# Performance work log

Hardware: AMD Instinct MI355X
Metric: run time of the kernel (lower is better)

## Reference

```python
import jax, jax.numpy as jnp
import numpy as np

N_NODES = 50000
DEG = 16
N_EDGES = N_NODES * DEG  # 800000
C_IN = 64
C_OUT = 64


def setup_inputs() -> dict:
    key = jax.random.key(0)
    k_x, k_src, k_ea, k_w, k_b = jax.random.split(key, 5)
    x = jax.random.normal(k_x, (N_NODES, C_IN), dtype=jnp.float32)
    # Every node appears DEG times as a destination -> no empty segments in max-aggregation.
    dst = jnp.repeat(jnp.arange(N_NODES, dtype=jnp.int32), DEG)
    src = jax.random.randint(k_src, (N_EDGES,), 0, N_NODES, dtype=jnp.int32)
    edge_index = jnp.stack([src, dst], axis=0)  # [2, E], row0=source(j), row1=target(i)
    edge_attr = jax.random.normal(k_ea, (N_EDGES, 1), dtype=jnp.float32)  # unused by forward (faithful to source)
    # MLP(2*C_IN -> C_OUT): Linear weight [out, 2*in] + bias, kaiming-ish scale
    W = jax.random.normal(k_w, (C_OUT, 2 * C_IN), dtype=jnp.float32) * (1.0 / np.sqrt(2 * C_IN))
    b = jax.random.normal(k_b, (C_OUT,), dtype=jnp.float32) * 0.01
    return {"x": x, "edge_index": edge_index, "edge_attr": edge_attr, "W": W, "b": b}


def reference(x, edge_index, edge_attr, W, b):
    # PyG EdgeConv: out_i = max_{j in N(i)} MLP(concat(x_i, x_j - x_i)); aggr='max'
    src = edge_index[0]  # j (source)
    dst = edge_index[1]  # i (target)
    x_i = x[dst]                      # [E, C]
    x_j = x[src]                      # [E, C]
    feat = jnp.concatenate([x_i, x_j - x_i], axis=-1)   # [E, 2C]
    msg = jax.nn.relu(feat @ W.T + b)                    # [E, C_out] per-edge MLP
    out = jax.ops.segment_max(msg, dst, num_segments=x.shape[0])  # scatter-max
    # Guard against -inf for isolated nodes (none by construction, but match scatter fill=0)
    return jnp.where(jnp.isneginf(out), 0.0, out)
```

## Files before the change

### kernel.cpp

```cpp
#include <hip/hip_runtime.h>


#define DEG 16
#define C 64
#define NPW 8
#define WPB 4

typedef __attribute__((ext_vector_type(8))) short s16x8;
typedef __attribute__((ext_vector_type(4))) float f32x4;

__device__ __forceinline__ unsigned short f2bf(float f) {
    union { float f; unsigned u; } v; v.f = f;
    unsigned u = v.u + 0x7FFFu + ((v.u >> 16) & 1u);
    return (unsigned short)(u >> 16);
}


__global__ __launch_bounds__(256) void prep(const float* __restrict__ x,
                                            const float* __restrict__ W,
                                            unsigned short* __restrict__ ws_u,
                                            int n4) {
    int i = blockIdx.x * blockDim.x + threadIdx.x;
    if (i < n4) {
        f32x4 v = ((const f32x4*)x)[i];
        ushort4 o;
        o.x = f2bf(v[0]); o.y = f2bf(v[1]); o.z = f2bf(v[2]); o.w = f2bf(v[3]);
        ((ushort4*)ws_u)[i] = o;
    }
    if (blockIdx.x == 0 && threadIdx.x < 64) {
        const int lane = threadIdx.x, col = lane & 15, quad = lane >> 4;
        unsigned short* wf = ws_u + (size_t)n4 * 4;
        #pragma unroll
        for (int nt = 0; nt < 4; ++nt) {
            const float* wrow = W + (nt * 16 + col) * (2 * C);
            #pragma unroll
            for (int ks = 0; ks < 2; ++ks) {
                const int k0 = ks * 32 + quad * 8;
                f32x4 w1a = *(const f32x4*)(wrow + k0);
                f32x4 w1b = *(const f32x4*)(wrow + k0 + 4);
                f32x4 w2a = *(const f32x4*)(wrow + C + k0);
                f32x4 w2b = *(const f32x4*)(wrow + C + k0 + 4);
                s16x8 t2, td;
                #pragma unroll
                for (int j = 0; j < 4; ++j) {
                    t2[j]     = (short)f2bf(w2a[j]);
                    t2[j + 4] = (short)f2bf(w2b[j]);
                    td[j]     = (short)f2bf(w1a[j] - w2a[j]);
                    td[j + 4] = (short)f2bf(w1b[j] - w2b[j]);
                }
                *(s16x8*)(wf + (((0 * 8) + nt * 2 + ks) * 64 + lane) * 8) = td;
                *(s16x8*)(wf + (((1 * 8) + nt * 2 + ks) * 64 + lane) * 8) = t2;
            }
        }
    }
}

__global__ __launch_bounds__(256, 3) void edgeconv_mfma(
    const unsigned short* __restrict__ xb,
    const int* __restrict__ src,
    const float* __restrict__ bias,
    float* __restrict__ out,
    int n_groups, int n_nodes)
{
    const int lane = threadIdx.x & 63;
    const int wave = threadIdx.x >> 6;
    const int col  = lane & 15;
    const int quad = lane >> 4;
    int group = blockIdx.x * WPB + wave;
    if (group >= n_groups) group = n_groups - 1;
    const int node0 = group * NPW;

    int idx[NPW];
    #pragma unroll
    for (int n = 0; n < NPW; ++n)
        idx[n] = src[node0 * DEG + n * DEG + col];

    const unsigned short* wf = xb + (size_t)n_nodes * C;
    s16x8 bd[4][2], b2[4][2];
    #pragma unroll
    for (int nt = 0; nt < 4; ++nt)
        #pragma unroll
        for (int ks = 0; ks < 2; ++ks) {
            bd[nt][ks] = *(const s16x8*)(wf + ((nt * 2 + ks) * 64 + lane) * 8);
            b2[nt][ks] = *(const s16x8*)(wf + ((8 + nt * 2 + ks) * 64 + lane) * 8);
        }

    const int xirow = node0 + (col & 7);
    s16x8 xi0 = *(const s16x8*)(xb + xirow * C + quad * 8);
    s16x8 xi1 = *(const s16x8*)(xb + xirow * C + 32 + quad * 8);
    f32x4 baseD[4];
    #pragma unroll
    for (int nt = 0; nt < 4; ++nt) {
        float bv = bias[nt * 16 + col];
        baseD[nt] = (f32x4){bv, bv, bv, bv};
    }
    #pragma unroll
    for (int nt = 0; nt < 4; ++nt) {
        baseD[nt] = __builtin_amdgcn_mfma_f32_16x16x32_bf16(xi0, bd[nt][0], baseD[nt], 0, 0, 0);
        baseD[nt] = __builtin_amdgcn_mfma_f32_16x16x32_bf16(xi1, bd[nt][1], baseD[nt], 0, 0, 0);
    }

    s16x8 xa[NPW][2];
    #pragma unroll
    for (int n = 0; n < NPW; ++n) {
        xa[n][0] = *(const s16x8*)(xb + idx[n] * C + quad * 8);
        xa[n][1] = *(const s16x8*)(xb + idx[n] * C + 32 + quad * 8);
    }

    #pragma unroll
    for (int n = 0; n < NPW; ++n) {
        const int slane = ((n >> 2) << 4) | col;
        f32x4 acc[4];
        #pragma unroll
        for (int nt = 0; nt < 4; ++nt) {
            float bb = __shfl(baseD[nt][n & 3], slane);
            acc[nt] = (f32x4){bb, bb, bb, bb};
        }
        #pragma unroll
        for (int nt = 0; nt < 4; ++nt) {
            acc[nt] = __builtin_amdgcn_mfma_f32_16x16x32_bf16(xa[n][0], b2[nt][0], acc[nt], 0, 0, 0);
            acc[nt] = __builtin_amdgcn_mfma_f32_16x16x32_bf16(xa[n][1], b2[nt][1], acc[nt], 0, 0, 0);
        }
        float m[4];
        #pragma unroll
        for (int nt = 0; nt < 4; ++nt) {
            float t = fmaxf(fmaxf(acc[nt][0], acc[nt][1]),
                            fmaxf(acc[nt][2], acc[nt][3]));
            t = fmaxf(t, __shfl_xor(t, 16));
            t = fmaxf(t, __shfl_xor(t, 32));
            m[nt] = t;
        }
        float r = quad == 0 ? m[0] : quad == 1 ? m[1] : quad == 2 ? m[2] : m[3];
        r = fmaxf(r, 0.0f);
        out[(node0 + n) * C + lane] = r;
    }
}

__global__ __launch_bounds__(256, 2) void edgeconv_fallback(
    const float* __restrict__ x, const int* __restrict__ src,
    const float* __restrict__ W, const float* __restrict__ bias,
    float* __restrict__ out, int n_groups)
{
    const int lane = threadIdx.x & 63, wave = threadIdx.x >> 6;
    const int col = lane & 15, quad = lane >> 4;
    int group = blockIdx.x * WPB + wave;
    if (group >= n_groups) group = n_groups - 1;

    auto frag = [&](int row, int koff) {
        const float* p = x + row * C + koff;
        f32x4 a = *(const f32x4*)p, b = *(const f32x4*)(p + 4);
        s16x8 r;
        #pragma unroll
        for (int j = 0; j < 4; ++j) {
            r[j] = (short)f2bf(a[j]); r[j + 4] = (short)f2bf(b[j]);
        }
        return r;
    };

    s16x8 b2[4][2];
    f32x4 baseD[4];
    {
        s16x8 bd[4][2];
        #pragma unroll
        for (int nt = 0; nt < 4; ++nt) {
            const float* wrow = W + (nt * 16 + col) * (2 * C);
            #pragma unroll
            for (int ks = 0; ks < 2; ++ks) {
                const int k0 = ks * 32 + quad * 8;
                f32x4 w1a = *(const f32x4*)(wrow + k0);
                f32x4 w1b = *(const f32x4*)(wrow + k0 + 4);
                f32x4 w2a = *(const f32x4*)(wrow + C + k0);
                f32x4 w2b = *(const f32x4*)(wrow + C + k0 + 4);
                s16x8 t2, td;
                #pragma unroll
                for (int j = 0; j < 4; ++j) {
                    t2[j] = (short)f2bf(w2a[j]); t2[j + 4] = (short)f2bf(w2b[j]);
                    td[j] = (short)f2bf(w1a[j] - w2a[j]);
                    td[j + 4] = (short)f2bf(w1b[j] - w2b[j]);
                }
                b2[nt][ks] = t2; bd[nt][ks] = td;
            }
        }
        #pragma unroll
        for (int nt = 0; nt < 4; ++nt) {
            float bv = bias[nt * 16 + col];
            baseD[nt] = (f32x4){bv, bv, bv, bv};
        }
        const int nrow = group * 16 + col;
        s16x8 xi0 = frag(nrow, quad * 8), xi1 = frag(nrow, 32 + quad * 8);
        #pragma unroll
        for (int nt = 0; nt < 4; ++nt) {
            baseD[nt] = __builtin_amdgcn_mfma_f32_16x16x32_bf16(xi0, bd[nt][0], baseD[nt], 0, 0, 0);
            baseD[nt] = __builtin_amdgcn_mfma_f32_16x16x32_bf16(xi1, bd[nt][1], baseD[nt], 0, 0, 0);
        }
    }
    int idx[16];
    #pragma unroll
    for (int n = 0; n < 16; ++n) idx[n] = src[group * 256 + n * DEG + col];
    s16x8 xa[3][2];
    #pragma unroll
    for (int p = 0; p < 2; ++p) {
        xa[p][0] = frag(idx[p], quad * 8); xa[p][1] = frag(idx[p], 32 + quad * 8);
    }
    #pragma unroll
    for (int n = 0; n < 16; ++n) {
        if (n + 2 < 16) {
            xa[(n + 2) % 3][0] = frag(idx[n + 2], quad * 8);
            xa[(n + 2) % 3][1] = frag(idx[n + 2], 32 + quad * 8);
        }
        const int slane = ((n >> 2) << 4) | col;
        f32x4 acc[4];
        #pragma unroll
        for (int nt = 0; nt < 4; ++nt) {
            float bb = __shfl(baseD[nt][n & 3], slane);
            acc[nt] = (f32x4){bb, bb, bb, bb};
        }
        #pragma unroll
        for (int nt = 0; nt < 4; ++nt) {
            acc[nt] = __builtin_amdgcn_mfma_f32_16x16x32_bf16(xa[n % 3][0], b2[nt][0], acc[nt], 0, 0, 0);
            acc[nt] = __builtin_amdgcn_mfma_f32_16x16x32_bf16(xa[n % 3][1], b2[nt][1], acc[nt], 0, 0, 0);
        }
        float m[4];
        #pragma unroll
        for (int nt = 0; nt < 4; ++nt) {
            float t = fmaxf(fmaxf(acc[nt][0], acc[nt][1]),
                            fmaxf(acc[nt][2], acc[nt][3]));
            t = fmaxf(t, __shfl_xor(t, 16));
            t = fmaxf(t, __shfl_xor(t, 32));
            m[nt] = t;
        }
        float r = quad == 0 ? m[0] : quad == 1 ? m[1] : quad == 2 ? m[2] : m[3];
        out[(group * 16 + n) * C + lane] = fmaxf(r, 0.0f);
    }
}

extern "C" void kernel_launch(void* const* d_in, const int* in_sizes, int n_in,
                              void* d_out, int out_size, void* d_ws, size_t ws_size,
                              hipStream_t stream) {
    const float* x    = (const float*)d_in[0];
    const int*   src  = (const int*)  d_in[1];
    const float* W    = (const float*)d_in[3];
    const float* b    = (const float*)d_in[4];
    float*       out  = (float*)d_out;

    const int n_nodes = in_sizes[0] / C;
    const size_t need = ((size_t)n_nodes * C + 16 * 64 * 8) * sizeof(unsigned short);

    if (ws_size >= need) {
        unsigned short* ws_u = (unsigned short*)d_ws;
        const int n4 = n_nodes * C / 4;
        const int n_groups = (n_nodes + NPW - 1) / NPW;
        const int grid = (n_groups + WPB - 1) / WPB;
        prep<<<(n4 + 255) / 256, 256, 0, stream>>>(x, W, ws_u, n4);
        edgeconv_mfma<<<grid, 256, 0, stream>>>(ws_u, src, b, out, n_groups, n_nodes);
    } else {
        const int n_groups = (n_nodes + 15) / 16;
        edgeconv_fallback<<<(n_groups + WPB - 1) / WPB, 256, 0, stream>>>(
            x, src, W, b, out, n_groups);
    }
}
```

Measured before the change: 98.38 us.

## Precompute per-node linear projections, then gather-max fp16 rows per edge

Uses linearity: W2·x_j is computed once per node, and the base term (W1-W2)·x_i+b is computed once per destination, both stored as fp16. The edge stage then only gathers the projected source rows, takes an elementwise max, adds the base and applies relu, because relu(base + y) is monotone in y. This removes the per-edge MFMA work (16x redundant GEMM) and replaces it with a gather of 128-byte fp16 rows. It adds an fp16 rounding step on the intermediates, which may cost accuracy.

Result: slower. 104.6 us (+6.3%).

```diff
diff --git a/kernel.cpp b/kernel.cpp
--- a/kernel.cpp
+++ b/kernel.cpp
@@ -3,11 +3,12 @@
 
 #define DEG 16
 #define C 64
-#define NPW 8
 #define WPB 4
 
 typedef __attribute__((ext_vector_type(8))) short s16x8;
 typedef __attribute__((ext_vector_type(4))) float f32x4;
+typedef __attribute__((ext_vector_type(4))) int   i32x4;
+typedef _Float16 h8 __attribute__((ext_vector_type(8)));
 
 __device__ __forceinline__ unsigned short f2bf(float f) {
     union { float f; unsigned u; } v; v.f = f;
@@ -15,125 +16,135 @@
     return (unsigned short)(u >> 16);
 }
 
-
-__global__ __launch_bounds__(256) void prep(const float* __restrict__ x,
-                                            const float* __restrict__ W,
-                                            unsigned short* __restrict__ ws_u,
-                                            int n4) {
-    int i = blockIdx.x * blockDim.x + threadIdx.x;
-    if (i < n4) {
-        f32x4 v = ((const f32x4*)x)[i];
-        ushort4 o;
-        o.x = f2bf(v[0]); o.y = f2bf(v[1]); o.z = f2bf(v[2]); o.w = f2bf(v[3]);
-        ((ushort4*)ws_u)[i] = o;
-    }
-    if (blockIdx.x == 0 && threadIdx.x < 64) {
-        const int lane = threadIdx.x, col = lane & 15, quad = lane >> 4;
-        unsigned short* wf = ws_u + (size_t)n4 * 4;
-        #pragma unroll
-        for (int nt = 0; nt < 4; ++nt) {
-            const float* wrow = W + (nt * 16 + col) * (2 * C);
-            #pragma unroll
-            for (int ks = 0; ks < 2; ++ks) {
-                const int k0 = ks * 32 + quad * 8;
-                f32x4 w1a = *(const f32x4*)(wrow + k0);
-                f32x4 w1b = *(const f32x4*)(wrow + k0 + 4);
-                f32x4 w2a = *(const f32x4*)(wrow + C + k0);
-                f32x4 w2b = *(const f32x4*)(wrow + C + k0 + 4);
-                s16x8 t2, td;
-                #pragma unroll
-                for (int j = 0; j < 4; ++j) {
-                    t2[j]     = (short)f2bf(w2a[j]);
-                    t2[j + 4] = (short)f2bf(w2b[j]);
-                    td[j]     = (short)f2bf(w1a[j] - w2a[j]);
-                    td[j + 4] = (short)f2bf(w1b[j] - w2b[j]);
-                }
-                *(s16x8*)(wf + (((0 * 8) + nt * 2 + ks) * 64 + lane) * 8) = td;
-                *(s16x8*)(wf + (((1 * 8) + nt * 2 + ks) * 64 + lane) * 8) = t2;
-            }
-        }
-    }
-}
-
-__global__ __launch_bounds__(256, 3) void edgeconv_mfma(
-    const unsigned short* __restrict__ xb,
-    const int* __restrict__ src,
+__global__ __launch_bounds__(256) void prep_gemm(
+    const float* __restrict__ x, const float* __restrict__ W,
     const float* __restrict__ bias,
-    float* __restrict__ out,
+    _Float16* __restrict__ y, _Float16* __restrict__ base,
     int n_groups, int n_nodes)
 {
     const int lane = threadIdx.x & 63;
     const int wave = threadIdx.x >> 6;
     const int col  = lane & 15;
     const int quad = lane >> 4;
+    int g = blockIdx.x * WPB + wave;
+    if (g >= n_groups) g = n_groups - 1;
+
+    s16x8 bd[4][2], b2[4][2];
+    #pragma unroll
+    for (int nt = 0; nt < 4; ++nt) {
+        const float* wrow = W + (size_t)(nt * 16 + col) * (2 * C);
+        #pragma unroll
+        for (int ks = 0; ks < 2; ++ks) {
+            const int k0 = ks * 32 + quad * 8;
+            f32x4 w1a = *(const f32x4*)(wrow + k0);
+            f32x4 w1b = *(const f32x4*)(wrow + k0 + 4);
+            f32x4 w2a = *(const f32x4*)(wrow + C + k0);
+            f32x4 w2b = *(const f32x4*)(wrow + C + k0 + 4);
+            s16x8 t2, td;
+            #pragma unroll
+            for (int j = 0; j < 4; ++j) {
+                t2[j]     = (short)f2bf(w2a[j]);
+                t2[j + 4] = (short)f2bf(w2b[j]);
+                td[j]     = (short)f2bf(w1a[j] - w2a[j]);
+                td[j + 4] = (short)f2bf(w1b[j] - w2b[j]);
+            }
+            bd[nt][ks] = td;
+            b2[nt][ks] = t2;
+        }
+    }
+
+    int arow = g * 16 + col;
+    if (arow >= n_nodes) arow = n_nodes - 1;
+    const float* xr = x + (size_t)arow * C;
+    f32x4 xa0 = __builtin_nontemporal_load((const f32x4*)(xr + quad * 8));
+    f32x4 xa1 = __builtin_nontemporal_load((const f32x4*)(xr + quad * 8 + 4));
+    f32x4 xb0 = __builtin_nontemporal_load((const f32x4*)(xr + 32 + quad * 8));
+    f32x4 xb1 = __builtin_nontemporal_load((const f32x4*)(xr + 32 + quad * 8 + 4));
+    s16x8 xi0, xi1;
+    #pragma unroll
+    for (int j = 0; j < 4; ++j) {
+        xi0[j]     = (short)f2bf(xa0[j]);
+        xi0[j + 4] = (short)f2bf(xa1[j]);
+        xi1[j]     = (short)f2bf(xb0[j]);
+        xi1[j + 4] = (short)f2bf(xb1[j]);
+    }
+
+    f32x4 yD[4], bD[4];
+    #pragma unroll
+    for (int nt = 0; nt < 4; ++nt) {
+        float bv = bias[nt * 16 + col];
+        bD[nt] = (f32x4){bv, bv, bv, bv};
+        yD[nt] = (f32x4){0.f, 0.f, 0.f, 0.f};
+    }
+    #pragma unroll
+    for (int nt = 0; nt < 4; ++nt) {
+        yD[nt] = __builtin_amdgcn_mfma_f32_16x16x32_bf16(xi0, b2[nt][0], yD[nt], 0, 0, 0);
+        yD[nt] = __builtin_amdgcn_mfma_f32_16x16x32_bf16(xi1, b2[nt][1], yD[nt], 0, 0, 0);
+        bD[nt] = __builtin_amdgcn_mfma_f32_16x16x32_bf16(xi0, bd[nt][0], bD[nt], 0, 0, 0);
+        bD[nt] = __builtin_amdgcn_mfma_f32_16x16x32_bf16(xi1, bd[nt][1], bD[nt], 0, 0, 0);
+    }
+
+    #pragma unroll
+    for (int nt = 0; nt < 4; ++nt) {
+        #pragma unroll
+        for (int reg = 0; reg < 4; ++reg) {
+            int orow = g * 16 + quad * 4 + reg;
+            if (orow < n_nodes) {
+                size_t o = (size_t)orow * C + nt * 16 + col;
+                y[o]    = (_Float16)yD[nt][reg];
+                base[o] = (_Float16)bD[nt][reg];
+            }
+        }
+    }
+}
+
+__global__ __launch_bounds__(256, 4) void edge_max(
+    const _Float16* __restrict__ y, const _Float16* __restrict__ base,
+    const int* __restrict__ src, float* __restrict__ out,
+    int n_groups, int n_nodes)
+{
+    const int lane = threadIdx.x & 63;
+    const int wave = threadIdx.x >> 6;
     int group = blockIdx.x * WPB + wave;
     if (group >= n_groups) group = n_groups - 1;
-    const int node0 = group * NPW;
-
-    int idx[NPW];
-    #pragma unroll
-    for (int n = 0; n < NPW; ++n)
-        idx[n] = src[node0 * DEG + n * DEG + col];
-
-    const unsigned short* wf = xb + (size_t)n_nodes * C;
-    s16x8 bd[4][2], b2[4][2];
-    #pragma unroll
-    for (int nt = 0; nt < 4; ++nt)
-        #pragma unroll
-        for (int ks = 0; ks < 2; ++ks) {
-            bd[nt][ks] = *(const s16x8*)(wf + ((nt * 2 + ks) * 64 + lane) * 8);
-            b2[nt][ks] = *(const s16x8*)(wf + ((8 + nt * 2 + ks) * 64 + lane) * 8);
-        }
-
-    const int xirow = node0 + (col & 7);
-    s16x8 xi0 = *(const s16x8*)(xb + xirow * C + quad * 8);
-    s16x8 xi1 = *(const s16x8*)(xb + xirow * C + 32 + quad * 8);
-    f32x4 baseD[4];
-    #pragma unroll
-    for (int nt = 0; nt < 4; ++nt) {
-        float bv = bias[nt * 16 + col];
-        baseD[nt] = (f32x4){bv, bv, bv, bv};
-    }
-    #pragma unroll
-    for (int nt = 0; nt < 4; ++nt) {
-        baseD[nt] = __builtin_amdgcn_mfma_f32_16x16x32_bf16(xi0, bd[nt][0], baseD[nt], 0, 0, 0);
-        baseD[nt] = __builtin_amdgcn_mfma_f32_16x16x32_bf16(xi1, bd[nt][1], baseD[nt], 0, 0, 0);
-    }
-
-    s16x8 xa[NPW][2];
-    #pragma unroll
-    for (int n = 0; n < NPW; ++n) {
-        xa[n][0] = *(const s16x8*)(xb + idx[n] * C + quad * 8);
-        xa[n][1] = *(const s16x8*)(xb + idx[n] * C + 32 + quad * 8);
-    }
-
-    #pragma unroll
-    for (int n = 0; n < NPW; ++n) {
-        const int slane = ((n >> 2) << 4) | col;
-        f32x4 acc[4];
-        #pragma unroll
-        for (int nt = 0; nt < 4; ++nt) {
-            float bb = __shfl(baseD[nt][n & 3], slane);
-            acc[nt] = (f32x4){bb, bb, bb, bb};
-        }
-        #pragma unroll
-        for (int nt = 0; nt < 4; ++nt) {
-            acc[nt] = __builtin_amdgcn_mfma_f32_16x16x32_bf16(xa[n][0], b2[nt][0], acc[nt], 0, 0, 0);
-            acc[nt] = __builtin_amdgcn_mfma_f32_16x16x32_bf16(xa[n][1], b2[nt][1], acc[nt], 0, 0, 0);
-        }
-        float m[4];
-        #pragma unroll
-        for (int nt = 0; nt < 4; ++nt) {
-            float t = fmaxf(fmaxf(acc[nt][0], acc[nt][1]),
-                            fmaxf(acc[nt][2], acc[nt][3]));
-            t = fmaxf(t, __shfl_xor(t, 16));
-            t = fmaxf(t, __shfl_xor(t, 32));
-            m[nt] = t;
-        }
-        float r = quad == 0 ? m[0] : quad == 1 ? m[1] : quad == 2 ? m[2] : m[3];
-        r = fmaxf(r, 0.0f);
-        out[(node0 + n) * C + lane] = r;
-    }
+    const int nloc = lane >> 3;
+    const int seg  = lane & 7;
+    int node = group * 8 + nloc;
+    if (node >= n_nodes) node = n_nodes - 1;
+
+    const i32x4* sp = (const i32x4*)(src + (size_t)node * DEG);
+    i32x4 ia = __builtin_nontemporal_load(sp + 0);
+    i32x4 ib = __builtin_nontemporal_load(sp + 1);
+    i32x4 ic = __builtin_nontemporal_load(sp + 2);
+    i32x4 id4 = __builtin_nontemporal_load(sp + 3);
+    int id[16] = {ia[0], ia[1], ia[2], ia[3], ib[0], ib[1], ib[2], ib[3],
+                  ic[0], ic[1], ic[2], ic[3], id4[0], id4[1], id4[2], id4[3]};
+
+    h8 r[16];
+    #pragma unroll
+    for (int e = 0; e < 16; ++e)
+        r[e] = *(const h8*)(y + (size_t)id[e] * C + seg * 8);
+
+    #pragma unroll
+    for (int e = 0; e < 8; ++e) r[e] = __builtin_elementwise_max(r[e], r[e + 8]);
+    #pragma unroll
+    for (int e = 0; e < 4; ++e) r[e] = __builtin_elementwise_max(r[e], r[e + 4]);
+    #pragma unroll
+    for (int e = 0; e < 2; ++e) r[e] = __builtin_elementwise_max(r[e], r[e + 2]);
+    r[0] = __builtin_elementwise_max(r[0], r[1]);
+
+    h8 bs = __builtin_nontemporal_load((const h8*)(base + (size_t)node * C + seg * 8));
+
+    float o[8];
+    #pragma unroll
+    for (int j = 0; j < 8; ++j)
+        o[j] = fmaxf((float)r[0][j] + (float)bs[j], 0.0f);
+
+    float* op = out + (size_t)node * C + seg * 8;
+    f32x4 o0 = (f32x4){o[0], o[1], o[2], o[3]};
+    f32x4 o1 = (f32x4){o[4], o[5], o[6], o[7]};
+    __builtin_nontemporal_store(o0, (f32x4*)op);
+    __builtin_nontemporal_store(o1, (f32x4*)op + 1);
 }
 
 __global__ __launch_bounds__(256, 2) void edgeconv_fallback(
@@ -147,7 +158,7 @@
     if (group >= n_groups) group = n_groups - 1;
 
     auto frag = [&](int row, int koff) {
-        const float* p = x + row * C + koff;
+        const float* p = x + (size_t)row * C + koff;
         f32x4 a = *(const f32x4*)p, b = *(const f32x4*)(p + 4);
         s16x8 r;
         #pragma unroll
@@ -163,7 +174,7 @@
         s16x8 bd[4][2];
         #pragma unroll
         for (int nt = 0; nt < 4; ++nt) {
-            const float* wrow = W + (nt * 16 + col) * (2 * C);
+            const float* wrow = W + (size_t)(nt * 16 + col) * (2 * C);
             #pragma unroll
             for (int ks = 0; ks < 2; ++ks) {
                 const int k0 = ks * 32 + quad * 8;
@@ -230,29 +241,29 @@
             m[nt] = t;
         }
         float r = quad == 0 ? m[0] : quad == 1 ? m[1] : quad == 2 ? m[2] : m[3];
-        out[(group * 16 + n) * C + lane] = fmaxf(r, 0.0f);
+        out[(size_t)(group * 16 + n) * C + lane] = fmaxf(r, 0.0f);
     }
 }
 
 extern "C" void kernel_launch(void* const* d_in, const int* in_sizes, int n_in,
                               void* d_out, int out_size, void* d_ws, size_t ws_size,
                               hipStream_t stream) {
-    const float* x    = (const float*)d_in[0];
-    const int*   src  = (const int*)  d_in[1];
-    const float* W    = (const float*)d_in[3];
-    const float* b    = (const float*)d_in[4];
-    float*       out  = (float*)d_out;
+    const float* x   = (const float*)d_in[0];
+    const int*   src = (const int*)  d_in[1];
+    const float* W   = (const float*)d_in[3];
+    const float* b   = (const float*)d_in[4];
+    float*       out = (float*)d_out;
 
     const int n_nodes = in_sizes[0] / C;
-    const size_t need = ((size_t)n_nodes * C + 16 * 64 * 8) * sizeof(unsigned short);
+    const size_t need = (size_t)n_nodes * C * 2 * sizeof(_Float16);
 
     if (ws_size >= need) {
-        unsigned short* ws_u = (unsigned short*)d_ws;
-        const int n4 = n_nodes * C / 4;
-        const int n_groups = (n_nodes + NPW - 1) / NPW;
-        const int grid = (n_groups + WPB - 1) / WPB;
-        prep<<<(n4 + 255) / 256, 256, 0, stream>>>(x, W, ws_u, n4);
-        edgeconv_mfma<<<grid, 256, 0, stream>>>(ws_u, src, b, out, n_groups, n_nodes);
+        _Float16* y    = (_Float16*)d_ws;
+        _Float16* base = y + (size_t)n_nodes * C;
+        const int g16 = (n_nodes + 15) / 16;
+        const int g8  = (n_nodes + 7) / 8;
+        prep_gemm<<<(g16 + WPB - 1) / WPB, 256, 0, stream>>>(x, W, b, y, base, g16, n_nodes);
+        edge_max<<<(g8 + WPB - 1) / WPB, 256, 0, stream>>>(y, base, src, out, g8, n_nodes);
     } else {
         const int n_groups = (n_nodes + 15) / 16;
         edgeconv_fallback<<<(n_groups + WPB - 1) / WPB, 256, 0, stream>>>(
```
